# Kernel tuning notes

Measured on AMD Instinct MI355X. Metric: run time of the kernel, lower is better.

Reference implementation:

```python
import jax, jax.numpy as jnp
import numpy as np

D_MODEL = 1024
N_HEADS = 16
D_K = D_MODEL // N_HEADS
D_FF = 4096
EPS = 1e-5


def _layernorm(x, g, b):
    mu = jnp.mean(x, axis=-1, keepdims=True)
    var = jnp.var(x, axis=-1, keepdims=True)
    return (x - mu) * jax.lax.rsqrt(var + EPS) * g + b


def setup_inputs() -> dict:
    key = jax.random.key(0)
    ks = jax.random.split(key, 12)
    s = 0.02
    x = jax.random.normal(ks[0], (2, 2048, D_MODEL), dtype=jnp.float32)
    # Linear weights stored [in, out] so y = x @ W + b
    wq = jax.random.normal(ks[1], (D_MODEL, D_MODEL), dtype=jnp.float32) * s
    wk = jax.random.normal(ks[2], (D_MODEL, D_MODEL), dtype=jnp.float32) * s
    wv = jax.random.normal(ks[3], (D_MODEL, D_MODEL), dtype=jnp.float32) * s
    wo = jax.random.normal(ks[4], (D_MODEL, D_MODEL), dtype=jnp.float32) * s
    bq = jnp.zeros((D_MODEL,), jnp.float32)
    bk = jnp.zeros((D_MODEL,), jnp.float32)
    bv = jnp.zeros((D_MODEL,), jnp.float32)
    bo = jnp.zeros((D_MODEL,), jnp.float32)
    ln1_g = jnp.ones((D_MODEL,), jnp.float32)
    ln1_b = jnp.zeros((D_MODEL,), jnp.float32)
    ln2_g = jnp.ones((D_MODEL,), jnp.float32)
    ln2_b = jnp.zeros((D_MODEL,), jnp.float32)
    w1 = jax.random.normal(ks[5], (D_MODEL, D_FF), dtype=jnp.float32) * s
    b1 = jnp.zeros((D_FF,), jnp.float32)
    w2 = jax.random.normal(ks[6], (D_FF, D_MODEL), dtype=jnp.float32) * s
    b2 = jnp.zeros((D_MODEL,), jnp.float32)
    return {"x": x, "wq": wq, "bq": bq, "wk": wk, "bk": bk, "wv": wv, "bv": bv,
            "wo": wo, "bo": bo, "ln1_g": ln1_g, "ln1_b": ln1_b,
            "ln2_g": ln2_g, "ln2_b": ln2_b, "w1": w1, "b1": b1, "w2": w2, "b2": b2}


def reference(x, wq, bq, wk, bk, wv, bv, wo, bo, ln1_g, ln1_b, ln2_g, ln2_b, w1, b1, w2, b2):
    B, S, _ = x.shape
    res = x
    # project and split heads: [B, S, H, Dk]
    q = (x @ wq + bq).reshape(B, S, N_HEADS, D_K)
    k = (x @ wk + bk).reshape(B, S, N_HEADS, D_K)
    v = (x @ wv + bv).reshape(B, S, N_HEADS, D_K)
    # full score matrix [B, H, Sq, Sk] (faithful to unfused original)
    scores = jnp.einsum('bqhd,bkhd->bhqk', q, k) / jnp.sqrt(jnp.float32(D_K))
    weights = jax.nn.softmax(scores, axis=-1)
    attn = jnp.einsum('bhqk,bkhd->bqhd', weights, v).reshape(B, S, D_MODEL)
    x = _layernorm(res + attn @ wo + bo, ln1_g, ln1_b)
    res = x
    h = jax.nn.relu(x @ w1 + b1)
    x = _layernorm(res + h @ w2 + b2, ln2_g, ln2_b)
    return x
```

## Files before the change

kernel.cpp:

```cpp
#include <hip/hip_runtime.h>
#include <hip/hip_bf16.h>
#include <stdint.h>


typedef __hip_bfloat16 bf16;
typedef short bf16x8 __attribute__((ext_vector_type(8)));
typedef float f32x4 __attribute__((ext_vector_type(4)));

#if __has_builtin(__builtin_amdgcn_exp2f)
#define EXP2F(x) __builtin_amdgcn_exp2f(x)
#else
#define EXP2F(x) exp2f(x)
#endif

__device__ __forceinline__ float bf2f_lo(unsigned u) { return __uint_as_float(u << 16); }
__device__ __forceinline__ float bf2f_hi(unsigned u) { return __uint_as_float(u & 0xffff0000u); }
__device__ __forceinline__ ushort f2bf(float f) {
  union { bf16 h; ushort u; } c; c.h = __float2bfloat16(f); return c.u;
}
__device__ __forceinline__ uint pk_bf16(float a, float b) {
  union { __hip_bfloat162 h2; uint u; } c;
  c.h2 = __float22bfloat162_rn(make_float2(a, b));
  return c.u;
}
__device__ __forceinline__ bool is_f32(const uint* probe) { return probe[0] == 0x3F800000u; }
__device__ __forceinline__ float ld_param(const void* p, size_t i, bool f32) {
  return f32 ? ((const float*)p)[i] : __bfloat162float(((const bf16*)p)[i]);
}

template <bool A_EXT, bool RES_EXT>
__device__ __forceinline__ void gemm_body(
    const void* __restrict__ Av, const ushort* __restrict__ BT,
    const void* __restrict__ bias, const void* __restrict__ res,
    void* __restrict__ C, int N_, int K_, int bm, int bn,
    int kb, int ke, int mode, const uint* probe) {
  __shared__ ushort Asm_[128 * 32];
  __shared__ ushort Bsm_[128 * 32];

  const bool F32 = is_f32(probe);
  const bool AF = A_EXT && F32;

  const int tid = threadIdx.x;
  const int wave = tid >> 6;
  const int lane = tid & 63;
  const int wm = wave & 1, wn = wave >> 1;

  const int r0 = tid >> 2;
  const int c0 = (tid & 3) * 8;
  const int dA0 = r0 * 32 + c0;
  const int dA1 = dA0 + 64 * 32;

  const size_t aRow0 = (size_t)(bm * 128 + r0) * K_;
  const size_t aRow1 = aRow0 + (size_t)64 * K_;
  const ushort* pB0 = BT + (size_t)(bn * 128 + r0) * K_ + c0;
  const ushort* pB1 = pB0 + (size_t)64 * K_;

  auto ld4 = [&](int kk, uint4& A0, uint4& A1, uint4& B0, uint4& B1) {
    if (AF) {
      const float* Af = (const float*)Av;
      const float4 f0 = *(const float4*)(Af + aRow0 + kk + c0);
      const float4 f1 = *(const float4*)(Af + aRow0 + kk + c0 + 4);
      const float4 g0 = *(const float4*)(Af + aRow1 + kk + c0);
      const float4 g1 = *(const float4*)(Af + aRow1 + kk + c0 + 4);
      A0.x = pk_bf16(f0.x, f0.y); A0.y = pk_bf16(f0.z, f0.w);
      A0.z = pk_bf16(f1.x, f1.y); A0.w = pk_bf16(f1.z, f1.w);
      A1.x = pk_bf16(g0.x, g0.y); A1.y = pk_bf16(g0.z, g0.w);
      A1.z = pk_bf16(g1.x, g1.y); A1.w = pk_bf16(g1.z, g1.w);
    } else {
      const ushort* Ab = (const ushort*)Av;
      A0 = *(const uint4*)(Ab + aRow0 + kk + c0);
      A1 = *(const uint4*)(Ab + aRow1 + kk + c0);
    }
    B0 = *(const uint4*)(pB0 + kk);
    B1 = *(const uint4*)(pB1 + kk);
  };

  f32x4 zero = {0.f, 0.f, 0.f, 0.f};
  f32x4 acc[4][4];
#pragma unroll
  for (int i = 0; i < 4; ++i)
#pragma unroll
    for (int j = 0; j < 4; ++j) acc[i][j] = zero;

  const int m16 = lane & 15;
  const int quad = lane >> 4;
  const int koff = quad * 8;

  uint4 a0, a1, b0, b1;
  ld4(kb, a0, a1, b0, b1);

  for (int k0 = kb; k0 < ke; k0 += 32) {
    __syncthreads();
    *(uint4*)&Asm_[dA0] = a0;
    *(uint4*)&Asm_[dA1] = a1;
    *(uint4*)&Bsm_[dA0] = b0;
    *(uint4*)&Bsm_[dA1] = b1;
    __syncthreads();

    if (k0 + 32 < ke) ld4(k0 + 32, a0, a1, b0, b1);

    bf16x8 af[4], bfr[4];
#pragma unroll
    for (int i = 0; i < 4; ++i)
      af[i] = *(const bf16x8*)&Asm_[(wm * 64 + i * 16 + m16) * 32 + koff];
#pragma unroll
    for (int j = 0; j < 4; ++j)
      bfr[j] = *(const bf16x8*)&Bsm_[(wn * 64 + j * 16 + m16) * 32 + koff];
#pragma unroll
    for (int i = 0; i < 4; ++i)
#pragma unroll
      for (int j = 0; j < 4; ++j)
        acc[i][j] = __builtin_amdgcn_mfma_f32_16x16x32_bf16(af[i], bfr[j], acc[i][j], 0, 0, 0);
  }

  const int row0 = bm * 128 + wm * 64;
  const int col0 = bn * 128 + wn * 64;
#pragma unroll
  for (int j = 0; j < 4; ++j) {
    const int col = col0 + j * 16 + m16;
    const float bv = (mode == 3) ? 0.f : ld_param(bias, col, F32);
#pragma unroll
    for (int i = 0; i < 4; ++i) {
#pragma unroll
      for (int r = 0; r < 4; ++r) {
        const int row = row0 + i * 16 + quad * 4 + r;
        float v = acc[i][j][r] + bv;
        if (mode == 1) v = fmaxf(v, 0.f);
        if (mode == 2) v += ld_param(res, (size_t)row * N_ + col, RES_EXT && F32);
        if (mode >= 2) ((float*)C)[(size_t)row * N_ + col] = v;
        else ((bf16*)C)[(size_t)row * N_ + col] = __float2bfloat16(v);
      }
    }
  }
}

__global__ __launch_bounds__(256) void gemm_qkv(
    const void* A, const ushort* BT0, const ushort* BT1, const ushort* BT2,
    const void* b0, const void* b1, const void* b2,
    bf16* C0, bf16* C1, bf16* C2, const uint* probe) {
  const int sel = blockIdx.y >> 3, bn = blockIdx.y & 7;
  const ushort* BT = sel == 0 ? BT0 : (sel == 1 ? BT1 : BT2);
  const void* bb = sel == 0 ? b0 : (sel == 1 ? b1 : b2);
  bf16* C = sel == 0 ? C0 : (sel == 1 ? C1 : C2);
  gemm_body<true, false>(A, BT, bb, nullptr, C, 1024, 1024, blockIdx.x, bn,
                         0, 1024, 0, probe);
}
__global__ __launch_bounds__(256) void gemm_wo_sk(
    const ushort* A, const ushort* BT, const void* bias, const void* res,
    float* C0, float* C1, const uint* probe) {
  const int kz = blockIdx.z;
  gemm_body<false, true>(A, BT, bias, res, kz ? C1 : C0, 1024, 1024,
                         blockIdx.x, blockIdx.y, kz * 512, kz * 512 + 512,
                         kz ? 3 : 2, probe);
}
__global__ __launch_bounds__(256) void gemm_ffn1(
    const ushort* A, const ushort* BT, const void* bias, bf16* C, const uint* probe) {
  gemm_body<false, false>(A, BT, bias, nullptr, C, 4096, 1024,
                          blockIdx.x, blockIdx.y, 0, 1024, 1, probe);
}
__global__ __launch_bounds__(256) void gemm_ffn2_sk(
    const ushort* A, const ushort* BT, const void* bias, const ushort* res,
    float* C0, float* C1, const uint* probe) {
  const int kz = blockIdx.z;
  gemm_body<false, false>(A, BT, bias, res, kz ? C1 : C0, 1024, 4096,
                          blockIdx.x, blockIdx.y, kz * 2048, kz * 2048 + 2048,
                          kz ? 3 : 2, probe);
}

__global__ __launch_bounds__(256) void transpose_all(
    const void* W0, const void* W1, const void* W2, const void* W3,
    const void* W4, const void* W5,
    ushort* D0, ushort* D1, ushort* D2, ushort* D3, ushort* D4, ushort* D5,
    const uint* probe) {
  const int z = blockIdx.z;
  if (z < 4 && blockIdx.x >= 32) return;
  int n0, k0, K_, N_;
  const void* W;
  ushort* D;
  if (z < 4) {
    n0 = blockIdx.x * 32; k0 = blockIdx.y * 32; K_ = 1024; N_ = 1024;
    W = z == 0 ? W0 : z == 1 ? W1 : z == 2 ? W2 : W3;
    D = z == 0 ? D0 : z == 1 ? D1 : z == 2 ? D2 : D3;
  } else if (z == 4) {
    n0 = blockIdx.x * 32; k0 = blockIdx.y * 32; K_ = 1024; N_ = 4096; W = W4; D = D4;
  } else {
    n0 = blockIdx.y * 32; k0 = blockIdx.x * 32; K_ = 4096; N_ = 1024; W = W5; D = D5;
  }
  const bool F32 = is_f32(probe);
  __shared__ ushort tile[32][33];
  const int tx = threadIdx.x & 31, ty = threadIdx.x >> 5;
#pragma unroll
  for (int i = 0; i < 32; i += 8) {
    const size_t src = (size_t)(k0 + ty + i) * N_ + n0 + tx;
    tile[ty + i][tx] = F32 ? f2bf(((const float*)W)[src]) : ((const ushort*)W)[src];
  }
  __syncthreads();
#pragma unroll
  for (int i = 0; i < 32; i += 8)
    D[(size_t)(n0 + ty + i) * K_ + k0 + tx] = tile[tx][ty + i];
}

template <bool OUT_EXT>
__global__ __launch_bounds__(256) void ln_kernel(
    const float* __restrict__ X, const float* __restrict__ P,
    const void* __restrict__ g, const void* __restrict__ bta,
    void* __restrict__ out, const uint* probe) {
  const bool F32 = is_f32(probe);
  const int row = blockIdx.x;
  const int tid = threadIdx.x;
  const float4 a = *(const float4*)(X + (size_t)row * 1024 + tid * 4);
  const float4 b = *(const float4*)(P + (size_t)row * 1024 + tid * 4);
  const float xv[4] = {a.x + b.x, a.y + b.y, a.z + b.z, a.w + b.w};
  float s = xv[0] + xv[1] + xv[2] + xv[3];
  float ss = xv[0] * xv[0] + xv[1] * xv[1] + xv[2] * xv[2] + xv[3] * xv[3];
#pragma unroll
  for (int o = 32; o > 0; o >>= 1) { s += __shfl_down(s, o); ss += __shfl_down(ss, o); }
  __shared__ float red[8];
  if ((tid & 63) == 0) { red[tid >> 6] = s; red[4 + (tid >> 6)] = ss; }
  __syncthreads();
  s = red[0] + red[1] + red[2] + red[3];
  ss = red[4] + red[5] + red[6] + red[7];
  const float mu = s * (1.f / 1024.f);
  const float rstd = rsqrtf(ss * (1.f / 1024.f) - mu * mu + 1e-5f);
#pragma unroll
  for (int i = 0; i < 4; ++i) {
    const size_t idx = (size_t)row * 1024 + tid * 4 + i;
    const float y = (xv[i] - mu) * rstd * ld_param(g, tid * 4 + i, F32) +
                    ld_param(bta, tid * 4 + i, F32);
    if (OUT_EXT && F32) ((float*)out)[idx] = y;
    else ((bf16*)out)[idx] = __float2bfloat16(y);
  }
}

__global__ __launch_bounds__(256) void attn_mfma(
    const ushort* __restrict__ Qm, const ushort* __restrict__ Km,
    const ushort* __restrict__ Vm, ushort* __restrict__ Om) {
  __shared__ ushort Ks[64 * 72];
  __shared__ ushort Vt[64 * 72];
  __shared__ ushort Pw[4][32 * 72];

  const int tid = threadIdx.x;
  const int wave = tid >> 6, lane = tid & 63;
  const int m16 = lane & 15, quad = lane >> 4;
  const int bb = blockIdx.z, h = blockIdx.y;
  const size_t hb = ((size_t)bb * 2048) * 1024 + h * 64;
  const int q0 = blockIdx.x * 128 + wave * 32;

  const float QS = 0.125f * 1.44269504f;
  bf16x8 qf[2][2];
#pragma unroll
  for (int i = 0; i < 2; ++i)
#pragma unroll
    for (int c = 0; c < 2; ++c) {
      const uint4 u = *(const uint4*)(Qm + hb + (size_t)(q0 + 16 * i + m16) * 1024 + c * 32 + quad * 8);
      const uint w[4] = {u.x, u.y, u.z, u.w};
      bf16x8 f;
#pragma unroll
      for (int j = 0; j < 4; ++j) {
        const uint p = pk_bf16(bf2f_lo(w[j]) * QS, bf2f_hi(w[j]) * QS);
        f[2 * j]     = (short)(p & 0xffffu);
        f[2 * j + 1] = (short)(p >> 16);
      }
      qf[i][c] = f;
    }

  f32x4 zero = {0.f, 0.f, 0.f, 0.f};
  f32x4 acc[2][4];
#pragma unroll
  for (int i = 0; i < 2; ++i)
#pragma unroll
    for (int j = 0; j < 4; ++j) acc[i][j] = zero;
  float lp[2][4] = {{0.f, 0.f, 0.f, 0.f}, {0.f, 0.f, 0.f, 0.f}};

  const int skey = tid >> 2;
  const int sd = (tid & 3) * 8;
  const int pp = tid & 31;
  const int dc = tid >> 5;
  const int ka_ = 16 * ((2 * pp) & 3) + ((2 * pp) >> 2);
  const int kb_ = 16 * ((2 * pp + 1) & 3) + ((2 * pp + 1) >> 2);
  const ushort* Kg = Km + hb;
  const ushort* Vg = Vm + hb;

  uint4 kr0, kr1, vr0, vr1;
  kr0 = *(const uint4*)(Kg + (size_t)skey * 1024 + sd);
  kr1 = *(const uint4*)(Kg + (size_t)skey * 1024 + sd + 32);
  vr0 = *(const uint4*)(Vg + (size_t)ka_ * 1024 + dc * 8);
  vr1 = *(const uint4*)(Vg + (size_t)kb_ * 1024 + dc * 8);

  for (int kt = 0; kt < 2048; kt += 64) {
    __syncthreads();
    *(uint4*)&Ks[skey * 72 + sd] = kr0;
    *(uint4*)&Ks[skey * 72 + sd + 32] = kr1;
    {
      const uint va[4] = {vr0.x, vr0.y, vr0.z, vr0.w};
      const uint vb[4] = {vr1.x, vr1.y, vr1.z, vr1.w};
#pragma unroll
      for (int j = 0; j < 8; ++j) {
        const uint lo = (j & 1) ? (va[j >> 1] >> 16) : (va[j >> 1] & 0xffffu);
        const uint hi = (j & 1) ? (vb[j >> 1] & 0xffff0000u) : (vb[j >> 1] << 16);
        *(uint*)&Vt[(dc * 8 + j) * 72 + 2 * pp] = lo | hi;
      }
    }
    __syncthreads();

    if (kt + 64 < 2048) {
      kr0 = *(const uint4*)(Kg + (size_t)(kt + 64 + skey) * 1024 + sd);
      kr1 = *(const uint4*)(Kg + (size_t)(kt + 64 + skey) * 1024 + sd + 32);
      vr0 = *(const uint4*)(Vg + (size_t)(kt + 64 + ka_) * 1024 + dc * 8);
      vr1 = *(const uint4*)(Vg + (size_t)(kt + 64 + kb_) * 1024 + dc * 8);
    }

    f32x4 s[2][4];
#pragma unroll
    for (int i = 0; i < 2; ++i)
#pragma unroll
      for (int jn = 0; jn < 4; ++jn) s[i][jn] = zero;
#pragma unroll
    for (int c = 0; c < 2; ++c) {
      bf16x8 kb4[4];
#pragma unroll
      for (int jn = 0; jn < 4; ++jn)
        kb4[jn] = *(const bf16x8*)&Ks[(jn * 16 + m16) * 72 + c * 32 + quad * 8];
#pragma unroll
      for (int i = 0; i < 2; ++i)
#pragma unroll
        for (int jn = 0; jn < 4; ++jn)
          s[i][jn] = __builtin_amdgcn_mfma_f32_16x16x32_bf16(qf[i][c], kb4[jn], s[i][jn], 0, 0, 0);
    }

#pragma unroll
    for (int i = 0; i < 2; ++i)
#pragma unroll
      for (int r = 0; r < 4; ++r) {
        const float p0 = EXP2F(s[i][0][r]);
        const float p1 = EXP2F(s[i][1][r]);
        const float p2 = EXP2F(s[i][2][r]);
        const float p3 = EXP2F(s[i][3][r]);
        lp[i][r] += (p0 + p1) + (p2 + p3);
        uint2 pk;
        pk.x = pk_bf16(p0, p1);
        pk.y = pk_bf16(p2, p3);
        *(uint2*)&Pw[wave][(16 * i + quad * 4 + r) * 72 + m16 * 4] = pk;
      }
    asm volatile("s_waitcnt lgkmcnt(0)" ::: "memory");

#pragma unroll
    for (int c = 0; c < 2; ++c) {
      bf16x8 pa[2], vb4[4];
#pragma unroll
      for (int i = 0; i < 2; ++i)
        pa[i] = *(const bf16x8*)&Pw[wave][(16 * i + m16) * 72 + c * 32 + quad * 8];
#pragma unroll
      for (int jd = 0; jd < 4; ++jd)
        vb4[jd] = *(const bf16x8*)&Vt[(jd * 16 + m16) * 72 + c * 32 + quad * 8];
#pragma unroll
      for (int i = 0; i < 2; ++i)
#pragma unroll
        for (int jd = 0; jd < 4; ++jd)
          acc[i][jd] = __builtin_amdgcn_mfma_f32_16x16x32_bf16(pa[i], vb4[jd], acc[i][jd], 0, 0, 0);
    }
  }

#pragma unroll
  for (int i = 0; i < 2; ++i)
#pragma unroll
    for (int r = 0; r < 4; ++r) {
      float l = lp[i][r];
      l += __shfl_xor(l, 1); l += __shfl_xor(l, 2);
      l += __shfl_xor(l, 4); l += __shfl_xor(l, 8);
      const float inv = 1.f / l;
      const size_t rowoff = hb + (size_t)(q0 + 16 * i + quad * 4 + r) * 1024;
#pragma unroll
      for (int jd = 0; jd < 4; ++jd)
        Om[rowoff + jd * 16 + m16] = f2bf(acc[i][jd][r] * inv);
    }
}

extern "C" void kernel_launch(void* const* d_in, const int* in_sizes, int n_in,
                              void* d_out, int out_size, void* d_ws, size_t ws_size,
                              hipStream_t stream) {
  const void* x   = d_in[0];
  const void* wq  = d_in[1];
  const void* bq  = d_in[2];
  const void* wk  = d_in[3];
  const void* bk  = d_in[4];
  const void* wv  = d_in[5];
  const void* bv  = d_in[6];
  const void* wo  = d_in[7];
  const void* bo  = d_in[8];
  const uint* probe = (const uint*)d_in[9];
  const void* ln1g = d_in[9];
  const void* ln1b = d_in[10];
  const void* ln2g = d_in[11];
  const void* ln2b = d_in[12];
  const void* w1  = d_in[13];
  const void* b1  = d_in[14];
  const void* w2  = d_in[15];
  const void* b2  = d_in[16];

  char* ws = (char*)d_ws;
  const size_t MB = 1ull << 20;
  ushort* wqT = (ushort*)(ws + 0 * MB);
  ushort* wkT = (ushort*)(ws + 2 * MB);
  ushort* wvT = (ushort*)(ws + 4 * MB);
  ushort* woT = (ushort*)(ws + 6 * MB);
  ushort* w1T = (ushort*)(ws + 8 * MB);
  ushort* w2T = (ushort*)(ws + 16 * MB);
  ushort* Qb  = (ushort*)(ws + 24 * MB);
  ushort* Kb  = (ushort*)(ws + 32 * MB);
  ushort* Vb  = (ushort*)(ws + 40 * MB);
  ushort* AO  = (ushort*)(ws + 72 * MB);
  float*  T1  = (float*)(ws + 24 * MB);
  float*  P1w = (float*)(ws + 40 * MB);
  ushort* X1  = (ushort*)(ws + 56 * MB);
  ushort* Hb  = (ushort*)(ws + 24 * MB);
  float*  T1b = (float*)(ws + 0 * MB);
  float*  P1b = (float*)(ws + 64 * MB);

  const dim3 blk(256);
  transpose_all<<<dim3(128, 32, 6), blk, 0, stream>>>(
      wq, wk, wv, wo, w1, w2, wqT, wkT, wvT, woT, w1T, w2T, probe);

  gemm_qkv<<<dim3(32, 24), blk, 0, stream>>>(x, wqT, wkT, wvT, bq, bk, bv,
                                             (bf16*)Qb, (bf16*)Kb, (bf16*)Vb, probe);
  attn_mfma<<<dim3(16, 16, 2), blk, 0, stream>>>(Qb, Kb, Vb, AO);
  gemm_wo_sk<<<dim3(32, 8, 2), blk, 0, stream>>>(AO, woT, bo, x, T1, P1w, probe);
  ln_kernel<false><<<dim3(4096), blk, 0, stream>>>(T1, P1w, ln1g, ln1b, X1, probe);
  gemm_ffn1<<<dim3(32, 32), blk, 0, stream>>>(X1, w1T, b1, (bf16*)Hb, probe);
  gemm_ffn2_sk<<<dim3(32, 8, 2), blk, 0, stream>>>(Hb, w2T, b2, X1, T1b, P1b, probe);
  ln_kernel<true><<<dim3(4096), blk, 0, stream>>>(T1b, P1b, ln2g, ln2b, d_out, probe);
}
```

Baseline: 396.3 us.

## Deepen GEMM K-step to 64 and halve attention query tile per block

The shared GEMM body now stages two 32-wide K slices per barrier pair, using doubled LDS buffers and two sets of prefetch registers. This halves the number of __syncthreads per K loop and keeps more global loads in flight. The attention kernel drops from 32 to 16 query rows per wave and 128 to 64 per block, and the grid doubles from 512 to 1024 blocks, which gives more parallelism and lower register pressure. In exchange, each K/V tile loaded into LDS is reused by half as many queries, so K/V global traffic doubles and the GEMM uses more LDS and registers.

```diff
diff --git a/kernel.cpp b/kernel.cpp
--- a/kernel.cpp
+++ b/kernel.cpp
@@ -34,8 +34,8 @@
     const void* __restrict__ bias, const void* __restrict__ res,
     void* __restrict__ C, int N_, int K_, int bm, int bn,
     int kb, int ke, int mode, const uint* probe) {
-  __shared__ ushort Asm_[128 * 32];
-  __shared__ ushort Bsm_[128 * 32];
+  __shared__ ushort Asm_[2][128 * 32];
+  __shared__ ushort Bsm_[2][128 * 32];
 
   const bool F32 = is_f32(probe);
   const bool AF = A_EXT && F32;
@@ -86,31 +86,41 @@
   const int quad = lane >> 4;
   const int koff = quad * 8;
 
-  uint4 a0, a1, b0, b1;
-  ld4(kb, a0, a1, b0, b1);
-
-  for (int k0 = kb; k0 < ke; k0 += 32) {
+  uint4 a[2][2], b[2][2];
+  ld4(kb,      a[0][0], a[0][1], b[0][0], b[0][1]);
+  ld4(kb + 32, a[1][0], a[1][1], b[1][0], b[1][1]);
+
+  for (int k0 = kb; k0 < ke; k0 += 64) {
     __syncthreads();
-    *(uint4*)&Asm_[dA0] = a0;
-    *(uint4*)&Asm_[dA1] = a1;
-    *(uint4*)&Bsm_[dA0] = b0;
-    *(uint4*)&Bsm_[dA1] = b1;
+#pragma unroll
+    for (int s = 0; s < 2; ++s) {
+      *(uint4*)&Asm_[s][dA0] = a[s][0];
+      *(uint4*)&Asm_[s][dA1] = a[s][1];
+      *(uint4*)&Bsm_[s][dA0] = b[s][0];
+      *(uint4*)&Bsm_[s][dA1] = b[s][1];
+    }
     __syncthreads();
 
-    if (k0 + 32 < ke) ld4(k0 + 32, a0, a1, b0, b1);
-
-    bf16x8 af[4], bfr[4];
-#pragma unroll
-    for (int i = 0; i < 4; ++i)
-      af[i] = *(const bf16x8*)&Asm_[(wm * 64 + i * 16 + m16) * 32 + koff];
-#pragma unroll
-    for (int j = 0; j < 4; ++j)
-      bfr[j] = *(const bf16x8*)&Bsm_[(wn * 64 + j * 16 + m16) * 32 + koff];
-#pragma unroll
-    for (int i = 0; i < 4; ++i)
+    if (k0 + 64 < ke) {
+      ld4(k0 + 64, a[0][0], a[0][1], b[0][0], b[0][1]);
+      ld4(k0 + 96, a[1][0], a[1][1], b[1][0], b[1][1]);
+    }
+
+#pragma unroll
+    for (int s = 0; s < 2; ++s) {
+      bf16x8 af[4], bfr[4];
+#pragma unroll
+      for (int i = 0; i < 4; ++i)
+        af[i] = *(const bf16x8*)&Asm_[s][(wm * 64 + i * 16 + m16) * 32 + koff];
 #pragma unroll
       for (int j = 0; j < 4; ++j)
-        acc[i][j] = __builtin_amdgcn_mfma_f32_16x16x32_bf16(af[i], bfr[j], acc[i][j], 0, 0, 0);
+        bfr[j] = *(const bf16x8*)&Bsm_[s][(wn * 64 + j * 16 + m16) * 32 + koff];
+#pragma unroll
+      for (int i = 0; i < 4; ++i)
+#pragma unroll
+        for (int j = 0; j < 4; ++j)
+          acc[i][j] = __builtin_amdgcn_mfma_f32_16x16x32_bf16(af[i], bfr[j], acc[i][j], 0, 0, 0);
+    }
   }
 
   const int row0 = bm * 128 + wm * 64;
@@ -237,40 +247,36 @@
     const ushort* __restrict__ Vm, ushort* __restrict__ Om) {
   __shared__ ushort Ks[64 * 72];
   __shared__ ushort Vt[64 * 72];
-  __shared__ ushort Pw[4][32 * 72];
+  __shared__ ushort Pw[4][16 * 72];
 
   const int tid = threadIdx.x;
   const int wave = tid >> 6, lane = tid & 63;
   const int m16 = lane & 15, quad = lane >> 4;
   const int bb = blockIdx.z, h = blockIdx.y;
   const size_t hb = ((size_t)bb * 2048) * 1024 + h * 64;
-  const int q0 = blockIdx.x * 128 + wave * 32;
+  const int q0 = blockIdx.x * 64 + wave * 16;
 
   const float QS = 0.125f * 1.44269504f;
-  bf16x8 qf[2][2];
-#pragma unroll
-  for (int i = 0; i < 2; ++i)
-#pragma unroll
-    for (int c = 0; c < 2; ++c) {
-      const uint4 u = *(const uint4*)(Qm + hb + (size_t)(q0 + 16 * i + m16) * 1024 + c * 32 + quad * 8);
-      const uint w[4] = {u.x, u.y, u.z, u.w};
-      bf16x8 f;
-#pragma unroll
-      for (int j = 0; j < 4; ++j) {
-        const uint p = pk_bf16(bf2f_lo(w[j]) * QS, bf2f_hi(w[j]) * QS);
-        f[2 * j]     = (short)(p & 0xffffu);
-        f[2 * j + 1] = (short)(p >> 16);
-      }
-      qf[i][c] = f;
-    }
+  bf16x8 qf[2];
+#pragma unroll
+  for (int c = 0; c < 2; ++c) {
+    const uint4 u = *(const uint4*)(Qm + hb + (size_t)(q0 + m16) * 1024 + c * 32 + quad * 8);
+    const uint w[4] = {u.x, u.y, u.z, u.w};
+    bf16x8 f;
+#pragma unroll
+    for (int j = 0; j < 4; ++j) {
+      const uint p = pk_bf16(bf2f_lo(w[j]) * QS, bf2f_hi(w[j]) * QS);
+      f[2 * j]     = (short)(p & 0xffffu);
+      f[2 * j + 1] = (short)(p >> 16);
+    }
+    qf[c] = f;
+  }
 
   f32x4 zero = {0.f, 0.f, 0.f, 0.f};
-  f32x4 acc[2][4];
-#pragma unroll
-  for (int i = 0; i < 2; ++i)
-#pragma unroll
-    for (int j = 0; j < 4; ++j) acc[i][j] = zero;
-  float lp[2][4] = {{0.f, 0.f, 0.f, 0.f}, {0.f, 0.f, 0.f, 0.f}};
+  f32x4 acc[4];
+#pragma unroll
+  for (int j = 0; j < 4; ++j) acc[j] = zero;
+  float lp[4] = {0.f, 0.f, 0.f, 0.f};
 
   const int skey = tid >> 2;
   const int sd = (tid & 3) * 8;
@@ -310,11 +316,9 @@
       vr1 = *(const uint4*)(Vg + (size_t)(kt + 64 + kb_) * 1024 + dc * 8);
     }
 
-    f32x4 s[2][4];
-#pragma unroll
-    for (int i = 0; i < 2; ++i)
-#pragma unroll
-      for (int jn = 0; jn < 4; ++jn) s[i][jn] = zero;
+    f32x4 s[4];
+#pragma unroll
+    for (int jn = 0; jn < 4; ++jn) s[jn] = zero;
 #pragma unroll
     for (int c = 0; c < 2; ++c) {
       bf16x8 kb4[4];
@@ -322,58 +326,48 @@
       for (int jn = 0; jn < 4; ++jn)
         kb4[jn] = *(const bf16x8*)&Ks[(jn * 16 + m16) * 72 + c * 32 + quad * 8];
 #pragma unroll
-      for (int i = 0; i < 2; ++i)
-#pragma unroll
-        for (int jn = 0; jn < 4; ++jn)
-          s[i][jn] = __builtin_amdgcn_mfma_f32_16x16x32_bf16(qf[i][c], kb4[jn], s[i][jn], 0, 0, 0);
-    }
-
-#pragma unroll
-    for (int i = 0; i < 2; ++i)
-#pragma unroll
-      for (int r = 0; r < 4; ++r) {
-        const float p0 = EXP2F(s[i][0][r]);
-        const float p1 = EXP2F(s[i][1][r]);
-        const float p2 = EXP2F(s[i][2][r]);
-        const float p3 = EXP2F(s[i][3][r]);
-        lp[i][r] += (p0 + p1) + (p2 + p3);
-        uint2 pk;
-        pk.x = pk_bf16(p0, p1);
-        pk.y = pk_bf16(p2, p3);
-        *(uint2*)&Pw[wave][(16 * i + quad * 4 + r) * 72 + m16 * 4] = pk;
-      }
+      for (int jn = 0; jn < 4; ++jn)
+        s[jn] = __builtin_amdgcn_mfma_f32_16x16x32_bf16(qf[c], kb4[jn], s[jn], 0, 0, 0);
+    }
+
+#pragma unroll
+    for (int r = 0; r < 4; ++r) {
+      const float p0 = EXP2F(s[0][r]);
+      const float p1 = EXP2F(s[1][r]);
+      const float p2 = EXP2F(s[2][r]);
+      const float p3 = EXP2F(s[3][r]);
+      lp[r] += (p0 + p1) + (p2 + p3);
+      uint2 pk;
+      pk.x = pk_bf16(p0, p1);
+      pk.y = pk_bf16(p2, p3);
+      *(uint2*)&Pw[wave][(quad * 4 + r) * 72 + m16 * 4] = pk;
+    }
     asm volatile("s_waitcnt lgkmcnt(0)" ::: "memory");
 
 #pragma unroll
     for (int c = 0; c < 2; ++c) {
-      bf16x8 pa[2], vb4[4];
-#pragma unroll
-      for (int i = 0; i < 2; ++i)
-        pa[i] = *(const bf16x8*)&Pw[wave][(16 * i + m16) * 72 + c * 32 + quad * 8];
+      bf16x8 pa, vb4[4];
+      pa = *(const bf16x8*)&Pw[wave][m16 * 72 + c * 32 + quad * 8];
 #pragma unroll
       for (int jd = 0; jd < 4; ++jd)
         vb4[jd] = *(const bf16x8*)&Vt[(jd * 16 + m16) * 72 + c * 32 + quad * 8];
 #pragma unroll
-      for (int i = 0; i < 2; ++i)
-#pragma unroll
-        for (int jd = 0; jd < 4; ++jd)
-          acc[i][jd] = __builtin_amdgcn_mfma_f32_16x16x32_bf16(pa[i], vb4[jd], acc[i][jd], 0, 0, 0);
-    }
-  }
-
-#pragma unroll
-  for (int i = 0; i < 2; ++i)
-#pragma unroll
-    for (int r = 0; r < 4; ++r) {
-      float l = lp[i][r];
-      l += __shfl_xor(l, 1); l += __shfl_xor(l, 2);
-      l += __shfl_xor(l, 4); l += __shfl_xor(l, 8);
-      const float inv = 1.f / l;
-      const size_t rowoff = hb + (size_t)(q0 + 16 * i + quad * 4 + r) * 1024;
-#pragma unroll
       for (int jd = 0; jd < 4; ++jd)
-        Om[rowoff + jd * 16 + m16] = f2bf(acc[i][jd][r] * inv);
-    }
+        acc[jd] = __builtin_amdgcn_mfma_f32_16x16x32_bf16(pa, vb4[jd], acc[jd], 0, 0, 0);
+    }
+  }
+
+#pragma unroll
+  for (int r = 0; r < 4; ++r) {
+    float l = lp[r];
+    l += __shfl_xor(l, 1); l += __shfl_xor(l, 2);
+    l += __shfl_xor(l, 4); l += __shfl_xor(l, 8);
+    const float inv = 1.f / l;
+    const size_t rowoff = hb + (size_t)(q0 + quad * 4 + r) * 1024;
+#pragma unroll
+    for (int jd = 0; jd < 4; ++jd)
+      Om[rowoff + jd * 16 + m16] = f2bf(acc[jd][r] * inv);
+  }
 }
 
 extern "C" void kernel_launch(void* const* d_in, const int* in_sizes, int n_in,
@@ -423,7 +417,7 @@
 
   gemm_qkv<<<dim3(32, 24), blk, 0, stream>>>(x, wqT, wkT, wvT, bq, bk, bv,
                                              (bf16*)Qb, (bf16*)Kb, (bf16*)Vb, probe);
-  attn_mfma<<<dim3(16, 16, 2), blk, 0, stream>>>(Qb, Kb, Vb, AO);
+  attn_mfma<<<dim3(32, 16, 2), blk, 0, stream>>>(Qb, Kb, Vb, AO);
   gemm_wo_sk<<<dim3(32, 8, 2), blk, 0, stream>>>(AO, woT, bo, x, T1, P1w, probe);
   ln_kernel<false><<<dim3(4096), blk, 0, stream>>>(T1, P1w, ln1g, ln1b, X1, probe);
   gemm_ffn1<<<dim3(32, 32), blk, 0, stream>>>(X1, w1T, b1, (bf16*)Hb, probe);
```

Result: slower. 710.2 us (+79.2%).
